# Optimization experiments

Hardware: AMD Instinct MI355X
Metric: run time of the kernel (lower is better)

## Reference

```python
import jax, jax.numpy as jnp
import numpy as np

DIM = 768
NUM_HEADS = 12
MLP_RATIO = 4.0
HIDDEN = int(DIM * MLP_RATIO)
EPS = 1e-6  # flax LayerNorm default


def setup_inputs() -> dict:
    key = jax.random.key(0)
    ks = jax.random.split(key, 8)
    d = DIM
    init = lambda k, shape, fan_in: jax.random.normal(k, shape, jnp.float32) * (fan_in ** -0.5)
    return {
        "x": jax.random.normal(ks[0], (8, 1024, d), jnp.float32),
        "ln1_scale": jnp.ones((d,), jnp.float32),
        "ln1_bias": jnp.zeros((d,), jnp.float32),
        "qkv_w": init(ks[1], (d, 3 * d), d),
        "qkv_b": jnp.zeros((3 * d,), jnp.float32),
        "proj_w": init(ks[2], (d, d), d),
        "proj_b": jnp.zeros((d,), jnp.float32),
        "ln2_scale": jnp.ones((d,), jnp.float32),
        "ln2_bias": jnp.zeros((d,), jnp.float32),
        "fc1_w": init(ks[3], (d, HIDDEN), d),
        "fc1_b": jnp.zeros((HIDDEN,), jnp.float32),
        "fc2_w": init(ks[4], (HIDDEN, d), HIDDEN),
        "fc2_b": jnp.zeros((d,), jnp.float32),
    }


def _layernorm(x, scale, bias):
    mu = jnp.mean(x, axis=-1, keepdims=True)
    var = jnp.mean(jnp.square(x - mu), axis=-1, keepdims=True)
    return (x - mu) * jax.lax.rsqrt(var + EPS) * scale + bias


def reference(x, ln1_scale, ln1_bias, qkv_w, qkv_b, proj_w, proj_b,
              ln2_scale, ln2_bias, fc1_w, fc1_b, fc2_w, fc2_b):
    b, n, d = x.shape
    h = NUM_HEADS
    hd = d // h
    scale = hd ** -0.5

    # --- attention (pre-norm) ---
    y = _layernorm(x, ln1_scale, ln1_bias)
    qkv = y @ qkv_w + qkv_b                      # [b, n, 3d]
    qkv = qkv.reshape(b, n, 3, h, hd).transpose(2, 0, 3, 1, 4)  # [3, b, h, n, hd]
    q, k, v = qkv[0], qkv[1], qkv[2]
    attn = jnp.einsum("bhqd,bhkd->bhqk", q, k) * scale
    attn = jax.nn.softmax(attn, axis=-1)
    o = jnp.einsum("bhqk,bhkd->bhqd", attn, v)   # [b, h, n, hd]
    o = o.transpose(0, 2, 1, 3).reshape(b, n, d)
    x = x + (o @ proj_w + proj_b)

    # --- MLP (pre-norm) ---
    y = _layernorm(x, ln2_scale, ln2_bias)
    y = jax.nn.gelu(y @ fc1_w + fc1_b)
    x = x + (y @ fc2_w + fc2_b)
    return x
```

## Files before the change

### kernel.cpp

```cpp
#include <hip/hip_runtime.h>
#include <hip/hip_bf16.h>
#include <math.h>


#define DIM 768
#define SEQ 1024
#define BATCH 8
#define NHEAD 12
#define HDIM 64
#define HID 3072
#define MTOK (BATCH * SEQ)

typedef __attribute__((ext_vector_type(8))) short short8;
typedef __attribute__((ext_vector_type(4))) short short4v;
typedef __attribute__((ext_vector_type(4))) float floatx4;

__device__ __forceinline__ short f2s(float x) {
  __hip_bfloat16 h = __float2bfloat16(x);
  return __builtin_bit_cast(short, h);
}
__device__ __forceinline__ float s2f(short s) {
  return __bfloat162float(__builtin_bit_cast(__hip_bfloat16, s));
}
__device__ __forceinline__ floatx4 zf4() {
  floatx4 v; v[0] = v[1] = v[2] = v[3] = 0.f; return v;
}
__device__ __forceinline__ float gelu_f(float x) {
  float z = 0.7978845608028654f * (x + 0.044715f * x * x * x);
  float u = __expf(2.f * z);
  return 0.5f * x * (2.f - 2.f / (u + 1.f));
}

__global__ __launch_bounds__(256) void pre_kernel(
    const float* __restrict__ w0, short* __restrict__ o0,
    const float* __restrict__ w1, short* __restrict__ o1,
    const float* __restrict__ w2, short* __restrict__ o2,
    const float* __restrict__ w3, short* __restrict__ o3,
    const float* __restrict__ x, const float* __restrict__ ls,
    const float* __restrict__ lb, short* __restrict__ y) {
  const int id = blockIdx.x;
  const int t = threadIdx.x;
  if (id < 6912) {
    __shared__ float tile[32][33];
    const float* in;
    short* out;
    int K, N, tid;
    if (id < 1728)      { in = w0; out = o0; K = DIM; N = 3 * DIM; tid = id; }
    else if (id < 2304) { in = w1; out = o1; K = DIM; N = DIM;     tid = id - 1728; }
    else if (id < 4608) { in = w2; out = o2; K = DIM; N = HID;     tid = id - 2304; }
    else                { in = w3; out = o3; K = HID; N = DIM;     tid = id - 4608; }
    const int ntx = N >> 5;
    const int n0 = (tid % ntx) * 32, k0 = (tid / ntx) * 32;
    const int tx = t & 31, ty = t >> 5;
#pragma unroll
    for (int i = 0; i < 4; ++i)
      tile[ty + i * 8][tx] = in[(size_t)(k0 + ty + i * 8) * N + n0 + tx];
    __syncthreads();
#pragma unroll
    for (int i = 0; i < 4; ++i)
      out[(size_t)(n0 + ty + i * 8) * K + k0 + tx] = f2s(tile[tx][ty + i * 8]);
  } else {
    const int row = id - 6912;
    const float* xr = x + (size_t)row * DIM;
    float v[3];
    float s1 = 0.f, s2 = 0.f;
#pragma unroll
    for (int j = 0; j < 3; ++j) {
      v[j] = xr[t + j * 256];
      s1 += v[j];
      s2 += v[j] * v[j];
    }
#pragma unroll
    for (int off = 32; off; off >>= 1) {
      s1 += __shfl_down(s1, off, 64);
      s2 += __shfl_down(s2, off, 64);
    }
    __shared__ float r1[4], r2[4], bc[2];
    const int wave = t >> 6, lane = t & 63;
    if (lane == 0) { r1[wave] = s1; r2[wave] = s2; }
    __syncthreads();
    if (t == 0) {
      float S1 = r1[0] + r1[1] + r1[2] + r1[3];
      float S2 = r2[0] + r2[1] + r2[2] + r2[3];
      float mu = S1 * (1.0f / DIM);
      float var = S2 * (1.0f / DIM) - mu * mu;
      bc[0] = mu;
      bc[1] = rsqrtf(fmaxf(var, 0.f) + 1e-6f);
    }
    __syncthreads();
    const float mu = bc[0], rstd = bc[1];
#pragma unroll
    for (int j = 0; j < 3; ++j) {
      const int idx = t + j * 256;
      y[(size_t)row * DIM + idx] = f2s((v[j] - mu) * rstd * ls[idx] + lb[idx]);
    }
  }
}

__global__ __launch_bounds__(256) void ln_kernel(const float* __restrict__ x,
                                                 const float* __restrict__ scale,
                                                 const float* __restrict__ bias,
                                                 short* __restrict__ y) {
  const int row = blockIdx.x;
  const int t = threadIdx.x;
  const float* xr = x + (size_t)row * DIM;
  float v[3];
  float s1 = 0.f, s2 = 0.f;
#pragma unroll
  for (int j = 0; j < 3; ++j) {
    v[j] = xr[t + j * 256];
    s1 += v[j];
    s2 += v[j] * v[j];
  }
#pragma unroll
  for (int off = 32; off; off >>= 1) {
    s1 += __shfl_down(s1, off, 64);
    s2 += __shfl_down(s2, off, 64);
  }
  __shared__ float r1[4], r2[4], bc[2];
  const int wave = t >> 6, lane = t & 63;
  if (lane == 0) { r1[wave] = s1; r2[wave] = s2; }
  __syncthreads();
  if (t == 0) {
    float S1 = r1[0] + r1[1] + r1[2] + r1[3];
    float S2 = r2[0] + r2[1] + r2[2] + r2[3];
    float mu = S1 * (1.0f / DIM);
    float var = S2 * (1.0f / DIM) - mu * mu;
    bc[0] = mu;
    bc[1] = rsqrtf(fmaxf(var, 0.f) + 1e-6f);
  }
  __syncthreads();
  const float mu = bc[0], rstd = bc[1];
#pragma unroll
  for (int j = 0; j < 3; ++j) {
    const int idx = t + j * 256;
    y[(size_t)row * DIM + idx] = f2s((v[j] - mu) * rstd * scale[idx] + bias[idx]);
  }
}

template <int ROWS, int THREADS>
__device__ __forceinline__ void stageT(const short* __restrict__ src, int ld,
                                       short* lds, int t) {
#pragma unroll
  for (int i = 0; i < (ROWS * 4) / THREADS; ++i) {
    const int S = i * THREADS + t;
    const int row = S >> 2;
    const int chunk = (S & 3) ^ ((row >> 1) & 3);
    const short* g = src + (size_t)row * ld + chunk * 8;
    const unsigned off = __builtin_amdgcn_readfirstlane((unsigned)((S & ~63) * 16));
    __builtin_amdgcn_global_load_lds(
        (const __attribute__((address_space(1))) void*)g,
        (__attribute__((address_space(3))) void*)((char*)lds + off), 16, 0, 0);
  }
}

template <int ROWS, int THREADS>
__device__ __forceinline__ void stage8(const short* __restrict__ src, int ld,
                                       short* lds, int t) {
#pragma unroll
  for (int i = 0; i < (ROWS * 8) / THREADS; ++i) {
    const int S = i * THREADS + t;
    const int row = S >> 3;
    const int chunk = (S & 7) ^ (row & 7);
    const short* g = src + (size_t)row * ld + chunk * 8;
    const unsigned off = __builtin_amdgcn_readfirstlane((unsigned)((S & ~63) * 16));
    __builtin_amdgcn_global_load_lds(
        (const __attribute__((address_space(1))) void*)g,
        (__attribute__((address_space(3))) void*)((char*)lds + off), 16, 0, 0);
  }
}

template <int MODE>
__global__ __launch_bounds__(256) void gemm_w192(
    const short* __restrict__ A, const short* __restrict__ Bt,
    const float* __restrict__ bias,
    short* __restrict__ outB,
    short* __restrict__ Qb, short* __restrict__ Kb, short* __restrict__ Vtb,
    int N, int K) {
  __shared__ __align__(16) short Asm[2][4096];
  __shared__ __align__(16) short Bsm[2][6144];
  const int t = threadIdx.x;
  const int lane = t & 63, w = t >> 6, quad = lane >> 4, l15 = lane & 15;

  const int nbx = gridDim.x;
  const int lid = blockIdx.y * nbx + blockIdx.x;
  const int xcd = lid & 7, local = lid >> 3;
  const int m0 = ((local / nbx) * 8 + xcd) * 128;
  const int n0 = (local % nbx) * 192;
  const int mb = (w & 1) * 64, nb = (w >> 1) * 96;

  floatx4 acc[4][6];
#pragma unroll
  for (int mi = 0; mi < 4; ++mi)
#pragma unroll
    for (int ni = 0; ni < 6; ++ni) acc[mi][ni] = zf4();

  stageT<128, 256>(A + (size_t)m0 * K, K, Asm[0], t);
  stageT<192, 256>(Bt + (size_t)n0 * K, K, Bsm[0], t);

  const int nk = K >> 5;
  for (int kt = 0; kt < nk; ++kt) {
    __syncthreads();
    const int cur = kt & 1;
    if (kt + 1 < nk) {
      stageT<128, 256>(A + (size_t)m0 * K + (kt + 1) * 32, K, Asm[cur ^ 1], t);
      stageT<192, 256>(Bt + (size_t)n0 * K + (kt + 1) * 32, K, Bsm[cur ^ 1], t);
    }
    short8 a[4], b[6];
#pragma unroll
    for (int mi = 0; mi < 4; ++mi) {
      const int r = mb + mi * 16 + l15;
      a[mi] = *(const short8*)(Asm[cur] + r * 32 + (quad ^ ((r >> 1) & 3)) * 8);
    }
#pragma unroll
    for (int ni = 0; ni < 6; ++ni) {
      const int r = nb + ni * 16 + l15;
      b[ni] = *(const short8*)(Bsm[cur] + r * 32 + (quad ^ ((r >> 1) & 3)) * 8);
    }
#pragma unroll
    for (int mi = 0; mi < 4; ++mi)
#pragma unroll
      for (int ni = 0; ni < 6; ++ni)
        acc[mi][ni] = __builtin_amdgcn_mfma_f32_16x16x32_bf16(a[mi], b[ni], acc[mi][ni], 0, 0, 0);
  }

#pragma unroll
  for (int mi = 0; mi < 4; ++mi) {
    const int row0 = m0 + mb + mi * 16 + quad * 4;
#pragma unroll
    for (int ni = 0; ni < 6; ++ni) {
      const int col = n0 + nb + ni * 16 + l15;
      const float bv = bias[col];
      float v[4];
#pragma unroll
      for (int r = 0; r < 4; ++r) v[r] = acc[mi][ni][r] + bv;
      if (MODE == 0) {
        const int bb = row0 >> 10;
        const int s0 = row0 & 1023;
        if (col < 1536) {
          const int cc = (col < 768) ? col : col - 768;
          const int h = cc >> 6, d = cc & 63;
          short* dst = (col < 768 ? Qb : Kb) + (size_t)(bb * NHEAD + h) * SEQ * HDIM;
#pragma unroll
          for (int r = 0; r < 4; ++r) dst[(size_t)(s0 + r) * HDIM + d] = f2s(v[r]);
        } else {
          const int cc = col - 1536;
          const int h = cc >> 6, d = cc & 63;
          short4v pv;
#pragma unroll
          for (int r = 0; r < 4; ++r) pv[r] = f2s(v[r]);
          *(short4v*)(Vtb + ((size_t)(bb * NHEAD + h) * HDIM + d) * SEQ + s0) = pv;
        }
      } else {
#pragma unroll
        for (int r = 0; r < 4; ++r)
          outB[(size_t)(row0 + r) * N + col] = f2s(gelu_f(v[r]));
      }
    }
  }
}

__global__ __launch_bounds__(128) void gemm_n64(
    const short* __restrict__ A, const short* __restrict__ Bt,
    const float* __restrict__ bias, const float* __restrict__ res,
    float* __restrict__ outF, int N, int K) {
  __shared__ __align__(16) short Asm[2][8192];
  __shared__ __align__(16) short Bsm[2][4096];
  const int t = threadIdx.x;
  const int lane = t & 63, w = t >> 6, quad = lane >> 4, l15 = lane & 15;

  const int nbx = gridDim.x;
  const int lid = blockIdx.y * nbx + blockIdx.x;
  const int xcd = lid & 7, local = lid >> 3;
  const int m0 = ((local / nbx) * 8 + xcd) * 128;
  const int n0 = (local % nbx) * 64;
  const int mb = w * 64;

  floatx4 acc[4][4];
#pragma unroll
  for (int mi = 0; mi < 4; ++mi)
#pragma unroll
    for (int ni = 0; ni < 4; ++ni) acc[mi][ni] = zf4();

  stage8<128, 128>(A + (size_t)m0 * K, K, Asm[0], t);
  stage8<64, 128>(Bt + (size_t)n0 * K, K, Bsm[0], t);

  const int nk = K >> 6;
  for (int kt = 0; kt < nk; ++kt) {
    __syncthreads();
    const int cur = kt & 1;
    if (kt + 1 < nk) {
      stage8<128, 128>(A + (size_t)m0 * K + (kt + 1) * 64, K, Asm[cur ^ 1], t);
      stage8<64, 128>(Bt + (size_t)n0 * K + (kt + 1) * 64, K, Bsm[cur ^ 1], t);
    }
#pragma unroll
    for (int ks = 0; ks < 2; ++ks) {
      short8 a[4], b[4];
#pragma unroll
      for (int mi = 0; mi < 4; ++mi) {
        const int r = mb + mi * 16 + l15;
        a[mi] = *(const short8*)(Asm[cur] + r * 64 + (((ks * 4 + quad) ^ (r & 7)) * 8));
      }
#pragma unroll
      for (int ni = 0; ni < 4; ++ni) {
        const int r = ni * 16 + l15;
        b[ni] = *(const short8*)(Bsm[cur] + r * 64 + (((ks * 4 + quad) ^ (r & 7)) * 8));
      }
#pragma unroll
      for (int mi = 0; mi < 4; ++mi)
#pragma unroll
        for (int ni = 0; ni < 4; ++ni)
          acc[mi][ni] = __builtin_amdgcn_mfma_f32_16x16x32_bf16(a[mi], b[ni], acc[mi][ni], 0, 0, 0);
    }
  }

#pragma unroll
  for (int mi = 0; mi < 4; ++mi) {
    const int row0 = m0 + mb + mi * 16 + quad * 4;
#pragma unroll
    for (int ni = 0; ni < 4; ++ni) {
      const int col = n0 + ni * 16 + l15;
      const float bv = bias[col];
#pragma unroll
      for (int r = 0; r < 4; ++r) {
        const size_t idx = (size_t)(row0 + r) * N + col;
        outF[idx] = acc[mi][ni][r] + bv + res[idx];
      }
    }
  }
}

__device__ __forceinline__ void stage64(const short* __restrict__ src, int ld,
                                        short* lds, int t) {
  const int lane = t & 63, w = t >> 6;
#pragma unroll
  for (int i = 0; i < 2; ++i) {
    const int S = w * 128 + i * 64 + lane;
    const int r = S >> 3, c0 = S & 7;
    const int c = c0 ^ (r & 7);
    const short* g = src + (size_t)r * ld + c * 8;
    const unsigned off = __builtin_amdgcn_readfirstlane((unsigned)((w * 128 + i * 64) * 16));
    __builtin_amdgcn_global_load_lds(
        (const __attribute__((address_space(1))) void*)g,
        (__attribute__((address_space(3))) void*)((char*)lds + off), 16, 0, 0);
  }
}

__global__ __launch_bounds__(256) void attn_kernel(
    const short* __restrict__ Qb, const short* __restrict__ Kb,
    const short* __restrict__ Vtb, short* __restrict__ o) {
  __shared__ __align__(16) short Ks[2][4096];
  __shared__ __align__(16) short Vts[2][4096];
  __shared__ __align__(16) short Pt[8192];
  const int t = threadIdx.x;
  const int lane = t & 63, w = t >> 6, quad = lane >> 4, l15 = lane & 15;
  const int bh = blockIdx.x;
  const int q0 = blockIdx.y * 128;
  const size_t qkbase = (size_t)bh * SEQ * HDIM;
  const size_t vbase = (size_t)bh * HDIM * SEQ;
  short* ptw = Pt + w * 2048;
  const float cexp = 0.18033688011f;

  short8 bq[2][2];
#pragma unroll
  for (int mi = 0; mi < 2; ++mi)
#pragma unroll
    for (int ks = 0; ks < 2; ++ks)
      bq[mi][ks] = *(const short8*)(Qb + qkbase +
                                    (size_t)(q0 + w * 32 + mi * 16 + l15) * HDIM +
                                    ks * 32 + quad * 8);

  floatx4 oacc[4][2];
  float l_acc[2] = {0.f, 0.f};
#pragma unroll
  for (int di = 0; di < 4; ++di)
#pragma unroll
    for (int mi = 0; mi < 2; ++mi) oacc[di][mi] = zf4();

  stage64(Kb + qkbase, HDIM, Ks[0], t);
  stage64(Vtb + vbase, SEQ, Vts[0], t);

  for (int kt = 0; kt < 16; ++kt) {
    __syncthreads();
    const int cur = kt & 1;
    if (kt < 15) {
      stage64(Kb + qkbase + (size_t)(kt + 1) * 64 * HDIM, HDIM, Ks[cur ^ 1], t);
      stage64(Vtb + vbase + (kt + 1) * 64, SEQ, Vts[cur ^ 1], t);
    }

    floatx4 sacc[4][2];
#pragma unroll
    for (int ni = 0; ni < 4; ++ni)
#pragma unroll
      for (int mi = 0; mi < 2; ++mi) sacc[ni][mi] = zf4();
#pragma unroll
    for (int ks = 0; ks < 2; ++ks) {
      short8 ak[4];
#pragma unroll
      for (int ni = 0; ni < 4; ++ni) {
        const int r = ni * 16 + l15;
        ak[ni] = *(const short8*)(Ks[cur] + r * 64 + (((ks * 4 + quad) ^ (r & 7)) * 8));
      }
#pragma unroll
      for (int ni = 0; ni < 4; ++ni)
#pragma unroll
        for (int mi = 0; mi < 2; ++mi)
          sacc[ni][mi] = __builtin_amdgcn_mfma_f32_16x16x32_bf16(ak[ni], bq[mi][ks], sacc[ni][mi], 0, 0, 0);
    }

#pragma unroll
    for (int mi = 0; mi < 2; ++mi) {
      const int row = mi * 16 + l15;
      const int swz = (row & 7) ^ ((row & 8) >> 1);
#pragma unroll
      for (int ni = 0; ni < 4; ++ni) {
        short4v pk;
#pragma unroll
        for (int r = 0; r < 4; ++r) {
          const float p = exp2f(sacc[ni][mi][r] * cexp);
          l_acc[mi] += p;
          pk[r] = f2s(p);
        }
        const int c = ni * 2 + (quad >> 1);
        *(short4v*)(ptw + row * 64 + ((c ^ swz) * 8 + (quad & 1) * 4)) = pk;
      }
    }

#pragma unroll
    for (int ks = 0; ks < 2; ++ks) {
      short8 bp[2];
#pragma unroll
      for (int mi = 0; mi < 2; ++mi) {
        const int row = mi * 16 + l15;
        const int swz = (row & 7) ^ ((row & 8) >> 1);
        bp[mi] = *(const short8*)(ptw + row * 64 + (((ks * 4 + quad) ^ swz) * 8));
      }
      short8 av[4];
#pragma unroll
      for (int di = 0; di < 4; ++di) {
        const int r = di * 16 + l15;
        av[di] = *(const short8*)(Vts[cur] + r * 64 + (((ks * 4 + quad) ^ (r & 7)) * 8));
      }
#pragma unroll
      for (int di = 0; di < 4; ++di)
#pragma unroll
        for (int mi = 0; mi < 2; ++mi)
          oacc[di][mi] = __builtin_amdgcn_mfma_f32_16x16x32_bf16(av[di], bp[mi], oacc[di][mi], 0, 0, 0);
    }
  }

  const int bb = bh / NHEAD, hh = bh % NHEAD;
  float inv[2];
#pragma unroll
  for (int mi = 0; mi < 2; ++mi) {
    float l = l_acc[mi];
    l += __shfl_xor(l, 16, 64);
    l += __shfl_xor(l, 32, 64);
    inv[mi] = 1.0f / l;
  }
#pragma unroll
  for (int di = 0; di < 4; ++di)
#pragma unroll
    for (int mi = 0; mi < 2; ++mi) {
      const int tok = bb * SEQ + q0 + w * 32 + mi * 16 + l15;
      const int d = hh * HDIM + di * 16 + quad * 4;
      short4v ov;
#pragma unroll
      for (int r = 0; r < 4; ++r) ov[r] = f2s(oacc[di][mi][r] * inv[mi]);
      *(short4v*)(o + (size_t)tok * DIM + d) = ov;
    }
}

extern "C" void kernel_launch(void* const* d_in, const int* in_sizes, int n_in,
                              void* d_out, int out_size, void* d_ws, size_t ws_size,
                              hipStream_t stream) {
  const float* x      = (const float*)d_in[0];
  const float* ln1_s  = (const float*)d_in[1];
  const float* ln1_b  = (const float*)d_in[2];
  const float* qkv_w  = (const float*)d_in[3];
  const float* qkv_b  = (const float*)d_in[4];
  const float* proj_w = (const float*)d_in[5];
  const float* proj_b = (const float*)d_in[6];
  const float* ln2_s  = (const float*)d_in[7];
  const float* ln2_b  = (const float*)d_in[8];
  const float* fc1_w  = (const float*)d_in[9];
  const float* fc1_b  = (const float*)d_in[10];
  const float* fc2_w  = (const float*)d_in[11];
  const float* fc2_b  = (const float*)d_in[12];
  float* out = (float*)d_out;

  char* p = (char*)d_ws;
  short* wqt = (short*)p; p += (size_t)(3 * DIM) * DIM * 2;
  short* wpt = (short*)p; p += (size_t)DIM * DIM * 2;
  short* w1t = (short*)p; p += (size_t)HID * DIM * 2;
  short* w2t = (short*)p; p += (size_t)DIM * HID * 2;
  short* y   = (short*)p; p += (size_t)MTOK * DIM * 2;
  short* Qb  = (short*)p; p += (size_t)MTOK * DIM * 2;
  short* Kb  = (short*)p; p += (size_t)MTOK * DIM * 2;
  short* Vtb = (short*)p; p += (size_t)MTOK * DIM * 2;
  float* x1  = (float*)p; p += (size_t)MTOK * DIM * 4;
  short* h   = (short*)p; p += (size_t)MTOK * HID * 2;
  short* obuf = y;
  short* y2   = Qb;

  pre_kernel<<<6912 + MTOK, 256, 0, stream>>>(qkv_w, wqt, proj_w, wpt, fc1_w, w1t,
                                              fc2_w, w2t, x, ln1_s, ln1_b, y);
  gemm_w192<0><<<dim3(12, 64), 256, 0, stream>>>(
      y, wqt, qkv_b, nullptr, Qb, Kb, Vtb, 3 * DIM, DIM);
  attn_kernel<<<dim3(BATCH * NHEAD, SEQ / 128), 256, 0, stream>>>(Qb, Kb, Vtb, obuf);
  gemm_n64<<<dim3(12, 64), 128, 0, stream>>>(
      obuf, wpt, proj_b, x, x1, DIM, DIM);
  ln_kernel<<<MTOK, 256, 0, stream>>>(x1, ln2_s, ln2_b, y2);
  gemm_w192<2><<<dim3(16, 64), 256, 0, stream>>>(
      y2, w1t, fc1_b, h, nullptr, nullptr, nullptr, HID, DIM);
  gemm_n64<<<dim3(12, 64), 128, 0, stream>>>(
      h, w2t, fc2_b, x1, out, DIM, HID);
}
```

Before: 356.7 us.

## Unify GEMMs into 256x128 triple-buffered 8-wave kernel with split staging

Replaces the two GEMM kernels (a 128x192 tile with 256 threads and a 128x64 tile with 128 threads) with one 512-thread, 256x128-tile GEMM used for all four projections. Global-to-LDS loads are triple-buffered two k-steps ahead, and each k-step is split into two halves with explicit barriers, vmcnt/lgkmcnt waits and s_setprio around the MFMA bursts, so loads interleave with compute. The larger tile raises data reuse per LDS byte. In exchange it launches far fewer blocks (e.g. 192 for proj/fc2) on a 256-CU part, which may underfill the GPU, and the hand-counted wait values risk subtle ordering errors.

```diff
diff --git a/kernel.cpp b/kernel.cpp
--- a/kernel.cpp
+++ b/kernel.cpp
@@ -138,15 +138,15 @@
   }
 }
 
-template <int ROWS, int THREADS>
-__device__ __forceinline__ void stageT(const short* __restrict__ src, int ld,
-                                       short* lds, int t) {
-#pragma unroll
-  for (int i = 0; i < (ROWS * 4) / THREADS; ++i) {
-    const int S = i * THREADS + t;
-    const int row = S >> 2;
-    const int chunk = (S & 3) ^ ((row >> 1) & 3);
-    const short* g = src + (size_t)row * ld + chunk * 8;
+template <int J0, int J1>
+__device__ __forceinline__ void stage512(const short* __restrict__ src, int ldK,
+                                         short* lds, int t) {
+#pragma unroll
+  for (int j = J0; j < J1; ++j) {
+    const int S = j * 512 + t;
+    const int row = S >> 3;
+    const int chunk = (S & 7) ^ (row & 7);
+    const short* g = src + (size_t)row * ldK + chunk * 8;
     const unsigned off = __builtin_amdgcn_readfirstlane((unsigned)((S & ~63) * 16));
     __builtin_amdgcn_global_load_lds(
         (const __attribute__((address_space(1))) void*)g,
@@ -154,82 +154,119 @@
   }
 }
 
-template <int ROWS, int THREADS>
-__device__ __forceinline__ void stage8(const short* __restrict__ src, int ld,
-                                       short* lds, int t) {
-#pragma unroll
-  for (int i = 0; i < (ROWS * 8) / THREADS; ++i) {
-    const int S = i * THREADS + t;
-    const int row = S >> 3;
-    const int chunk = (S & 7) ^ (row & 7);
-    const short* g = src + (size_t)row * ld + chunk * 8;
-    const unsigned off = __builtin_amdgcn_readfirstlane((unsigned)((S & ~63) * 16));
-    __builtin_amdgcn_global_load_lds(
-        (const __attribute__((address_space(1))) void*)g,
-        (__attribute__((address_space(3))) void*)((char*)lds + off), 16, 0, 0);
-  }
-}
-
 template <int MODE>
-__global__ __launch_bounds__(256) void gemm_w192(
+__global__ __launch_bounds__(512) void gemm256(
     const short* __restrict__ A, const short* __restrict__ Bt,
-    const float* __restrict__ bias,
-    short* __restrict__ outB,
+    const float* __restrict__ bias, const float* __restrict__ res,
+    float* __restrict__ outF, short* __restrict__ outB,
     short* __restrict__ Qb, short* __restrict__ Kb, short* __restrict__ Vtb,
     int N, int K) {
-  __shared__ __align__(16) short Asm[2][4096];
-  __shared__ __align__(16) short Bsm[2][6144];
+  __shared__ __align__(16) short Asm[3][16384];
+  __shared__ __align__(16) short Bsm[3][8192];
   const int t = threadIdx.x;
   const int lane = t & 63, w = t >> 6, quad = lane >> 4, l15 = lane & 15;
+  const int wm = w >> 1, wn = w & 1;
 
   const int nbx = gridDim.x;
   const int lid = blockIdx.y * nbx + blockIdx.x;
   const int xcd = lid & 7, local = lid >> 3;
-  const int m0 = ((local / nbx) * 8 + xcd) * 128;
-  const int n0 = (local % nbx) * 192;
-  const int mb = (w & 1) * 64, nb = (w >> 1) * 96;
-
-  floatx4 acc[4][6];
+  const int m0 = ((local / nbx) * 8 + xcd) * 256;
+  const int n0 = (local % nbx) * 128;
+
+  floatx4 acc[4][4];
 #pragma unroll
   for (int mi = 0; mi < 4; ++mi)
 #pragma unroll
-    for (int ni = 0; ni < 6; ++ni) acc[mi][ni] = zf4();
-
-  stageT<128, 256>(A + (size_t)m0 * K, K, Asm[0], t);
-  stageT<192, 256>(Bt + (size_t)n0 * K, K, Bsm[0], t);
-
-  const int nk = K >> 5;
+    for (int ni = 0; ni < 4; ++ni) acc[mi][ni] = zf4();
+
+  const int nk = K >> 6;
+  stage512<0, 4>(A + (size_t)m0 * K, K, Asm[0], t);
+  stage512<0, 2>(Bt + (size_t)n0 * K, K, Bsm[0], t);
+  stage512<0, 4>(A + (size_t)m0 * K + 64, K, Asm[1], t);
+  stage512<0, 2>(Bt + (size_t)n0 * K + 64, K, Bsm[1], t);
+  asm volatile("s_waitcnt vmcnt(6)" ::: "memory");
+  __builtin_amdgcn_s_barrier();
+
+  int sc = 0;
   for (int kt = 0; kt < nk; ++kt) {
-    __syncthreads();
-    const int cur = kt & 1;
-    if (kt + 1 < nk) {
-      stageT<128, 256>(A + (size_t)m0 * K + (kt + 1) * 32, K, Asm[cur ^ 1], t);
-      stageT<192, 256>(Bt + (size_t)n0 * K + (kt + 1) * 32, K, Bsm[cur ^ 1], t);
-    }
-    short8 a[4], b[6];
-#pragma unroll
-    for (int mi = 0; mi < 4; ++mi) {
-      const int r = mb + mi * 16 + l15;
-      a[mi] = *(const short8*)(Asm[cur] + r * 32 + (quad ^ ((r >> 1) & 3)) * 8);
-    }
-#pragma unroll
-    for (int ni = 0; ni < 6; ++ni) {
-      const int r = nb + ni * 16 + l15;
-      b[ni] = *(const short8*)(Bsm[cur] + r * 32 + (quad ^ ((r >> 1) & 3)) * 8);
-    }
-#pragma unroll
-    for (int mi = 0; mi < 4; ++mi)
-#pragma unroll
-      for (int ni = 0; ni < 6; ++ni)
-        acc[mi][ni] = __builtin_amdgcn_mfma_f32_16x16x32_bf16(a[mi], b[ni], acc[mi][ni], 0, 0, 0);
+    int ss = sc + 2; if (ss >= 3) ss -= 3;
+    const short* As = Asm[sc];
+    const short* Bs = Bsm[sc];
+    const bool stg = (kt + 2 < nk);
+    const int koff = (kt + 2) * 64;
+
+    short8 a0[2][2], bf[4][2];
+#pragma unroll
+    for (int mi = 0; mi < 2; ++mi)
+#pragma unroll
+      for (int ks = 0; ks < 2; ++ks) {
+        const int r = wm * 64 + mi * 16 + l15;
+        a0[mi][ks] = *(const short8*)(As + r * 64 + (((ks * 4 + quad) ^ (r & 7)) * 8));
+      }
+#pragma unroll
+    for (int ni = 0; ni < 4; ++ni)
+#pragma unroll
+      for (int ks = 0; ks < 2; ++ks) {
+        const int r = wn * 64 + ni * 16 + l15;
+        bf[ni][ks] = *(const short8*)(Bs + r * 64 + (((ks * 4 + quad) ^ (r & 7)) * 8));
+      }
+    if (stg) {
+      stage512<0, 2>(A + (size_t)m0 * K + koff, K, Asm[ss], t);
+      stage512<0, 1>(Bt + (size_t)n0 * K + koff, K, Bsm[ss], t);
+    }
+    __builtin_amdgcn_s_barrier();
+    asm volatile("s_waitcnt lgkmcnt(0)" ::: "memory");
+    __builtin_amdgcn_s_setprio(1);
+#pragma unroll
+    for (int ks = 0; ks < 2; ++ks)
+#pragma unroll
+      for (int mi = 0; mi < 2; ++mi)
+#pragma unroll
+        for (int ni = 0; ni < 4; ++ni)
+          acc[mi][ni] = __builtin_amdgcn_mfma_f32_16x16x32_bf16(
+              a0[mi][ks], bf[ni][ks], acc[mi][ni], 0, 0, 0);
+    __builtin_amdgcn_s_setprio(0);
+    __builtin_amdgcn_s_barrier();
+
+    short8 a1[2][2];
+#pragma unroll
+    for (int mi = 0; mi < 2; ++mi)
+#pragma unroll
+      for (int ks = 0; ks < 2; ++ks) {
+        const int r = wm * 64 + 32 + mi * 16 + l15;
+        a1[mi][ks] = *(const short8*)(As + r * 64 + (((ks * 4 + quad) ^ (r & 7)) * 8));
+      }
+    if (stg) {
+      stage512<2, 4>(A + (size_t)m0 * K + koff, K, Asm[ss], t);
+      stage512<1, 2>(Bt + (size_t)n0 * K + koff, K, Bsm[ss], t);
+    }
+    __builtin_amdgcn_s_barrier();
+    asm volatile("s_waitcnt lgkmcnt(0)" ::: "memory");
+    __builtin_amdgcn_s_setprio(1);
+#pragma unroll
+    for (int ks = 0; ks < 2; ++ks)
+#pragma unroll
+      for (int mi = 0; mi < 2; ++mi)
+#pragma unroll
+        for (int ni = 0; ni < 4; ++ni)
+          acc[2 + mi][ni] = __builtin_amdgcn_mfma_f32_16x16x32_bf16(
+              a1[mi][ks], bf[ni][ks], acc[2 + mi][ni], 0, 0, 0);
+    __builtin_amdgcn_s_setprio(0);
+    if (stg) {
+      asm volatile("s_waitcnt vmcnt(6)" ::: "memory");
+    } else {
+      asm volatile("s_waitcnt vmcnt(0)" ::: "memory");
+    }
+    __builtin_amdgcn_s_barrier();
+    sc = sc + 1; if (sc == 3) sc = 0;
   }
 
 #pragma unroll
   for (int mi = 0; mi < 4; ++mi) {
-    const int row0 = m0 + mb + mi * 16 + quad * 4;
-#pragma unroll
-    for (int ni = 0; ni < 6; ++ni) {
-      const int col = n0 + nb + ni * 16 + l15;
+    const int row0 = m0 + wm * 64 + mi * 16 + quad * 4;
+#pragma unroll
+    for (int ni = 0; ni < 4; ++ni) {
+      const int col = n0 + wn * 64 + ni * 16 + l15;
       const float bv = bias[col];
       float v[4];
 #pragma unroll
@@ -251,80 +288,16 @@
           for (int r = 0; r < 4; ++r) pv[r] = f2s(v[r]);
           *(short4v*)(Vtb + ((size_t)(bb * NHEAD + h) * HDIM + d) * SEQ + s0) = pv;
         }
+      } else if (MODE == 1) {
+#pragma unroll
+        for (int r = 0; r < 4; ++r) {
+          const size_t idx = (size_t)(row0 + r) * N + col;
+          outF[idx] = v[r] + res[idx];
+        }
       } else {
 #pragma unroll
         for (int r = 0; r < 4; ++r)
           outB[(size_t)(row0 + r) * N + col] = f2s(gelu_f(v[r]));
-      }
-    }
-  }
-}
-
-__global__ __launch_bounds__(128) void gemm_n64(
-    const short* __restrict__ A, const short* __restrict__ Bt,
-    const float* __restrict__ bias, const float* __restrict__ res,
-    float* __restrict__ outF, int N, int K) {
-  __shared__ __align__(16) short Asm[2][8192];
-  __shared__ __align__(16) short Bsm[2][4096];
-  const int t = threadIdx.x;
-  const int lane = t & 63, w = t >> 6, quad = lane >> 4, l15 = lane & 15;
-
-  const int nbx = gridDim.x;
-  const int lid = blockIdx.y * nbx + blockIdx.x;
-  const int xcd = lid & 7, local = lid >> 3;
-  const int m0 = ((local / nbx) * 8 + xcd) * 128;
-  const int n0 = (local % nbx) * 64;
-  const int mb = w * 64;
-
-  floatx4 acc[4][4];
-#pragma unroll
-  for (int mi = 0; mi < 4; ++mi)
-#pragma unroll
-    for (int ni = 0; ni < 4; ++ni) acc[mi][ni] = zf4();
-
-  stage8<128, 128>(A + (size_t)m0 * K, K, Asm[0], t);
-  stage8<64, 128>(Bt + (size_t)n0 * K, K, Bsm[0], t);
-
-  const int nk = K >> 6;
-  for (int kt = 0; kt < nk; ++kt) {
-    __syncthreads();
-    const int cur = kt & 1;
-    if (kt + 1 < nk) {
-      stage8<128, 128>(A + (size_t)m0 * K + (kt + 1) * 64, K, Asm[cur ^ 1], t);
-      stage8<64, 128>(Bt + (size_t)n0 * K + (kt + 1) * 64, K, Bsm[cur ^ 1], t);
-    }
-#pragma unroll
-    for (int ks = 0; ks < 2; ++ks) {
-      short8 a[4], b[4];
-#pragma unroll
-      for (int mi = 0; mi < 4; ++mi) {
-        const int r = mb + mi * 16 + l15;
-        a[mi] = *(const short8*)(Asm[cur] + r * 64 + (((ks * 4 + quad) ^ (r & 7)) * 8));
-      }
-#pragma unroll
-      for (int ni = 0; ni < 4; ++ni) {
-        const int r = ni * 16 + l15;
-        b[ni] = *(const short8*)(Bsm[cur] + r * 64 + (((ks * 4 + quad) ^ (r & 7)) * 8));
-      }
-#pragma unroll
-      for (int mi = 0; mi < 4; ++mi)
-#pragma unroll
-        for (int ni = 0; ni < 4; ++ni)
-          acc[mi][ni] = __builtin_amdgcn_mfma_f32_16x16x32_bf16(a[mi], b[ni], acc[mi][ni], 0, 0, 0);
-    }
-  }
-
-#pragma unroll
-  for (int mi = 0; mi < 4; ++mi) {
-    const int row0 = m0 + mb + mi * 16 + quad * 4;
-#pragma unroll
-    for (int ni = 0; ni < 4; ++ni) {
-      const int col = n0 + ni * 16 + l15;
-      const float bv = bias[col];
-#pragma unroll
-      for (int r = 0; r < 4; ++r) {
-        const size_t idx = (size_t)(row0 + r) * N + col;
-        outF[idx] = acc[mi][ni][r] + bv + res[idx];
       }
     }
   }
@@ -505,14 +478,14 @@
 
   pre_kernel<<<6912 + MTOK, 256, 0, stream>>>(qkv_w, wqt, proj_w, wpt, fc1_w, w1t,
                                               fc2_w, w2t, x, ln1_s, ln1_b, y);
-  gemm_w192<0><<<dim3(12, 64), 256, 0, stream>>>(
-      y, wqt, qkv_b, nullptr, Qb, Kb, Vtb, 3 * DIM, DIM);
+  gemm256<0><<<dim3(18, 32), 512, 0, stream>>>(
+      y, wqt, qkv_b, nullptr, nullptr, nullptr, Qb, Kb, Vtb, 3 * DIM, DIM);
   attn_kernel<<<dim3(BATCH * NHEAD, SEQ / 128), 256, 0, stream>>>(Qb, Kb, Vtb, obuf);
-  gemm_n64<<<dim3(12, 64), 128, 0, stream>>>(
-      obuf, wpt, proj_b, x, x1, DIM, DIM);
+  gemm256<1><<<dim3(6, 32), 512, 0, stream>>>(
+      obuf, wpt, proj_b, x, x1, nullptr, nullptr, nullptr, nullptr, DIM, DIM);
   ln_kernel<<<MTOK, 256, 0, stream>>>(x1, ln2_s, ln2_b, y2);
-  gemm_w192<2><<<dim3(16, 64), 256, 0, stream>>>(
-      y2, w1t, fc1_b, h, nullptr, nullptr, nullptr, HID, DIM);
-  gemm_n64<<<dim3(12, 64), 128, 0, stream>>>(
-      h, w2t, fc2_b, x1, out, DIM, HID);
-}
+  gemm256<2><<<dim3(24, 32), 512, 0, stream>>>(
+      y2, w1t, fc1_b, nullptr, nullptr, h, nullptr, nullptr, nullptr, HID, DIM);
+  gemm256<1><<<dim3(6, 32), 512, 0, stream>>>(
+      h, w2t, fc2_b, x1, out, nullptr, nullptr, nullptr, nullptr, DIM, HID);
+}
```

Result: slower. 365.2 us (+2.4%).

## Deepen GEMM LDS pipelines to four stages with explicit vmcnt waits

Applied to the files above, without the earlier changes.

Both GEMM kernels move from a double-buffered LDS pipeline with __syncthreads to a 4-buffer ring with three K-tiles prefetched ahead. Each iteration waits only for the oldest tile via a partial s_waitcnt vmcnt count before a raw barrier. The n64 kernel also drops its K=64 tile in favour of K=32 tiles with the stageT swizzle. The aim is to hide global-to-LDS load latency better, at the cost of more LDS per block, which may lower occupancy. The hand-counted vmcnt values must exactly match the number of loads issued per stage.

```diff
diff --git a/kernel.cpp b/kernel.cpp
--- a/kernel.cpp
+++ b/kernel.cpp
@@ -154,22 +154,6 @@
   }
 }
 
-template <int ROWS, int THREADS>
-__device__ __forceinline__ void stage8(const short* __restrict__ src, int ld,
-                                       short* lds, int t) {
-#pragma unroll
-  for (int i = 0; i < (ROWS * 8) / THREADS; ++i) {
-    const int S = i * THREADS + t;
-    const int row = S >> 3;
-    const int chunk = (S & 7) ^ (row & 7);
-    const short* g = src + (size_t)row * ld + chunk * 8;
-    const unsigned off = __builtin_amdgcn_readfirstlane((unsigned)((S & ~63) * 16));
-    __builtin_amdgcn_global_load_lds(
-        (const __attribute__((address_space(1))) void*)g,
-        (__attribute__((address_space(3))) void*)((char*)lds + off), 16, 0, 0);
-  }
-}
-
 template <int MODE>
 __global__ __launch_bounds__(256) void gemm_w192(
     const short* __restrict__ A, const short* __restrict__ Bt,
@@ -177,8 +161,8 @@
     short* __restrict__ outB,
     short* __restrict__ Qb, short* __restrict__ Kb, short* __restrict__ Vtb,
     int N, int K) {
-  __shared__ __align__(16) short Asm[2][4096];
-  __shared__ __align__(16) short Bsm[2][6144];
+  __shared__ __align__(16) short Asm[4][4096];
+  __shared__ __align__(16) short Bsm[4][6144];
   const int t = threadIdx.x;
   const int lane = t & 63, w = t >> 6, quad = lane >> 4, l15 = lane & 15;
 
@@ -195,33 +179,46 @@
 #pragma unroll
     for (int ni = 0; ni < 6; ++ni) acc[mi][ni] = zf4();
 
-  stageT<128, 256>(A + (size_t)m0 * K, K, Asm[0], t);
-  stageT<192, 256>(Bt + (size_t)n0 * K, K, Bsm[0], t);
-
+  const short* Ab = A + (size_t)m0 * K;
+  const short* Bb = Bt + (size_t)n0 * K;
   const int nk = K >> 5;
-  for (int kt = 0; kt < nk; ++kt) {
-    __syncthreads();
-    const int cur = kt & 1;
-    if (kt + 1 < nk) {
-      stageT<128, 256>(A + (size_t)m0 * K + (kt + 1) * 32, K, Asm[cur ^ 1], t);
-      stageT<192, 256>(Bt + (size_t)n0 * K + (kt + 1) * 32, K, Bsm[cur ^ 1], t);
-    }
-    short8 a[4], b[6];
-#pragma unroll
-    for (int mi = 0; mi < 4; ++mi) {
-      const int r = mb + mi * 16 + l15;
-      a[mi] = *(const short8*)(Asm[cur] + r * 32 + (quad ^ ((r >> 1) & 3)) * 8);
-    }
-#pragma unroll
-    for (int ni = 0; ni < 6; ++ni) {
-      const int r = nb + ni * 16 + l15;
-      b[ni] = *(const short8*)(Bsm[cur] + r * 32 + (quad ^ ((r >> 1) & 3)) * 8);
-    }
-#pragma unroll
-    for (int mi = 0; mi < 4; ++mi)
-#pragma unroll
-      for (int ni = 0; ni < 6; ++ni)
-        acc[mi][ni] = __builtin_amdgcn_mfma_f32_16x16x32_bf16(a[mi], b[ni], acc[mi][ni], 0, 0, 0);
+
+  stageT<128, 256>(Ab, K, Asm[0], t);       stageT<192, 256>(Bb, K, Bsm[0], t);
+  stageT<128, 256>(Ab + 32, K, Asm[1], t);  stageT<192, 256>(Bb + 32, K, Bsm[1], t);
+  stageT<128, 256>(Ab + 64, K, Asm[2], t);  stageT<192, 256>(Bb + 64, K, Bsm[2], t);
+
+#define W192_STEP(BUF) do { \
+  short8 a_[4], b_[6]; \
+  _Pragma("unroll") for (int mi = 0; mi < 4; ++mi) { \
+    const int r = mb + mi * 16 + l15; \
+    a_[mi] = *(const short8*)(Asm[BUF] + r * 32 + ((quad ^ ((r >> 1) & 3)) * 8)); \
+  } \
+  _Pragma("unroll") for (int ni = 0; ni < 6; ++ni) { \
+    const int r = nb + ni * 16 + l15; \
+    b_[ni] = *(const short8*)(Bsm[BUF] + r * 32 + ((quad ^ ((r >> 1) & 3)) * 8)); \
+  } \
+  _Pragma("unroll") for (int mi = 0; mi < 4; ++mi) \
+    _Pragma("unroll") for (int ni = 0; ni < 6; ++ni) \
+      acc[mi][ni] = __builtin_amdgcn_mfma_f32_16x16x32_bf16(a_[mi], b_[ni], acc[mi][ni], 0, 0, 0); \
+} while (0)
+
+#define W192_IT(J, BUF, NXT) do { \
+  if ((J) + 2 < nk)      asm volatile("s_waitcnt vmcnt(10)" ::: "memory"); \
+  else if ((J) + 1 < nk) asm volatile("s_waitcnt vmcnt(5)" ::: "memory"); \
+  else                   asm volatile("s_waitcnt vmcnt(0)" ::: "memory"); \
+  __builtin_amdgcn_s_barrier(); \
+  if ((J) + 3 < nk) { \
+    stageT<128, 256>(Ab + ((J) + 3) * 32, K, Asm[NXT], t); \
+    stageT<192, 256>(Bb + ((J) + 3) * 32, K, Bsm[NXT], t); \
+  } \
+  W192_STEP(BUF); \
+} while (0)
+
+  for (int kt = 0; kt < nk; kt += 4) {
+    W192_IT(kt + 0, 0, 3);
+    W192_IT(kt + 1, 1, 0);
+    W192_IT(kt + 2, 2, 1);
+    W192_IT(kt + 3, 3, 2);
   }
 
 #pragma unroll
@@ -264,8 +261,8 @@
     const short* __restrict__ A, const short* __restrict__ Bt,
     const float* __restrict__ bias, const float* __restrict__ res,
     float* __restrict__ outF, int N, int K) {
-  __shared__ __align__(16) short Asm[2][8192];
-  __shared__ __align__(16) short Bsm[2][4096];
+  __shared__ __align__(16) short Asm[4][4096];
+  __shared__ __align__(16) short Bsm[4][2048];
   const int t = threadIdx.x;
   const int lane = t & 63, w = t >> 6, quad = lane >> 4, l15 = lane & 15;
 
@@ -282,36 +279,46 @@
 #pragma unroll
     for (int ni = 0; ni < 4; ++ni) acc[mi][ni] = zf4();
 
-  stage8<128, 128>(A + (size_t)m0 * K, K, Asm[0], t);
-  stage8<64, 128>(Bt + (size_t)n0 * K, K, Bsm[0], t);
-
-  const int nk = K >> 6;
-  for (int kt = 0; kt < nk; ++kt) {
-    __syncthreads();
-    const int cur = kt & 1;
-    if (kt + 1 < nk) {
-      stage8<128, 128>(A + (size_t)m0 * K + (kt + 1) * 64, K, Asm[cur ^ 1], t);
-      stage8<64, 128>(Bt + (size_t)n0 * K + (kt + 1) * 64, K, Bsm[cur ^ 1], t);
-    }
-#pragma unroll
-    for (int ks = 0; ks < 2; ++ks) {
-      short8 a[4], b[4];
-#pragma unroll
-      for (int mi = 0; mi < 4; ++mi) {
-        const int r = mb + mi * 16 + l15;
-        a[mi] = *(const short8*)(Asm[cur] + r * 64 + (((ks * 4 + quad) ^ (r & 7)) * 8));
-      }
-#pragma unroll
-      for (int ni = 0; ni < 4; ++ni) {
-        const int r = ni * 16 + l15;
-        b[ni] = *(const short8*)(Bsm[cur] + r * 64 + (((ks * 4 + quad) ^ (r & 7)) * 8));
-      }
-#pragma unroll
-      for (int mi = 0; mi < 4; ++mi)
-#pragma unroll
-        for (int ni = 0; ni < 4; ++ni)
-          acc[mi][ni] = __builtin_amdgcn_mfma_f32_16x16x32_bf16(a[mi], b[ni], acc[mi][ni], 0, 0, 0);
-    }
+  const short* Ab = A + (size_t)m0 * K;
+  const short* Bb = Bt + (size_t)n0 * K;
+  const int nk = K >> 5;
+
+  stageT<128, 128>(Ab, K, Asm[0], t);       stageT<64, 128>(Bb, K, Bsm[0], t);
+  stageT<128, 128>(Ab + 32, K, Asm[1], t);  stageT<64, 128>(Bb + 32, K, Bsm[1], t);
+  stageT<128, 128>(Ab + 64, K, Asm[2], t);  stageT<64, 128>(Bb + 64, K, Bsm[2], t);
+
+#define N64_STEP(BUF) do { \
+  short8 a_[4], b_[4]; \
+  _Pragma("unroll") for (int mi = 0; mi < 4; ++mi) { \
+    const int r = mb + mi * 16 + l15; \
+    a_[mi] = *(const short8*)(Asm[BUF] + r * 32 + ((quad ^ ((r >> 1) & 3)) * 8)); \
+  } \
+  _Pragma("unroll") for (int ni = 0; ni < 4; ++ni) { \
+    const int r = ni * 16 + l15; \
+    b_[ni] = *(const short8*)(Bsm[BUF] + r * 32 + ((quad ^ ((r >> 1) & 3)) * 8)); \
+  } \
+  _Pragma("unroll") for (int mi = 0; mi < 4; ++mi) \
+    _Pragma("unroll") for (int ni = 0; ni < 4; ++ni) \
+      acc[mi][ni] = __builtin_amdgcn_mfma_f32_16x16x32_bf16(a_[mi], b_[ni], acc[mi][ni], 0, 0, 0); \
+} while (0)
+
+#define N64_IT(J, BUF, NXT) do { \
+  if ((J) + 2 < nk)      asm volatile("s_waitcnt vmcnt(12)" ::: "memory"); \
+  else if ((J) + 1 < nk) asm volatile("s_waitcnt vmcnt(6)" ::: "memory"); \
+  else                   asm volatile("s_waitcnt vmcnt(0)" ::: "memory"); \
+  __builtin_amdgcn_s_barrier(); \
+  if ((J) + 3 < nk) { \
+    stageT<128, 128>(Ab + ((J) + 3) * 32, K, Asm[NXT], t); \
+    stageT<64, 128>(Bb + ((J) + 3) * 32, K, Bsm[NXT], t); \
+  } \
+  N64_STEP(BUF); \
+} while (0)
+
+  for (int kt = 0; kt < nk; kt += 4) {
+    N64_IT(kt + 0, 0, 3);
+    N64_IT(kt + 1, 1, 0);
+    N64_IT(kt + 2, 2, 1);
+    N64_IT(kt + 3, 3, 2);
   }
 
 #pragma unroll
```

After: 423.1 us. 1.19x slower.

## Load GEMM A-operand fragments directly from global into registers, bypassing LDS

Applied to the files above, without the earlier changes.

In both GEMM kernels, each wave now loads its A-operand MFMA fragments straight from global memory into registers, double-buffered across k-steps. Only the B tile is still staged through LDS, and the k-loop is unrolled by two so the two buffers alternate with fixed indices. This removes the A LDS staging, its LDS footprint and the LDS reads, which may raise occupancy. In exchange, the global A loads are less coalesced (16-byte strided row reads), waves sharing A rows fetch them redundantly, more registers are live, and the loop assumes nk is even.

```diff
diff --git a/kernel.cpp b/kernel.cpp
--- a/kernel.cpp
+++ b/kernel.cpp
@@ -177,7 +177,6 @@
     short* __restrict__ outB,
     short* __restrict__ Qb, short* __restrict__ Kb, short* __restrict__ Vtb,
     int N, int K) {
-  __shared__ __align__(16) short Asm[2][4096];
   __shared__ __align__(16) short Bsm[2][6144];
   const int t = threadIdx.x;
   const int lane = t & 63, w = t >> 6, quad = lane >> 4, l15 = lane & 15;
@@ -189,39 +188,49 @@
   const int n0 = (local % nbx) * 192;
   const int mb = (w & 1) * 64, nb = (w >> 1) * 96;
 
+  const short* pa[4];
+#pragma unroll
+  for (int mi = 0; mi < 4; ++mi)
+    pa[mi] = A + (size_t)(m0 + mb + mi * 16 + l15) * K + quad * 8;
+
   floatx4 acc[4][6];
 #pragma unroll
   for (int mi = 0; mi < 4; ++mi)
 #pragma unroll
     for (int ni = 0; ni < 6; ++ni) acc[mi][ni] = zf4();
 
-  stageT<128, 256>(A + (size_t)m0 * K, K, Asm[0], t);
+#define W192_STEP(BUF, AR) do { \
+  short8 b_[6]; \
+  _Pragma("unroll") for (int ni = 0; ni < 6; ++ni) { \
+    const int r = nb + ni * 16 + l15; \
+    b_[ni] = *(const short8*)(Bsm[BUF] + r * 32 + ((quad ^ ((r >> 1) & 3)) * 8)); \
+  } \
+  _Pragma("unroll") for (int mi = 0; mi < 4; ++mi) \
+    _Pragma("unroll") for (int ni = 0; ni < 6; ++ni) \
+      acc[mi][ni] = __builtin_amdgcn_mfma_f32_16x16x32_bf16(AR[mi], b_[ni], acc[mi][ni], 0, 0, 0); \
+} while (0)
+
+  short8 a0[4], a1[4];
+#pragma unroll
+  for (int mi = 0; mi < 4; ++mi) a0[mi] = *(const short8*)(pa[mi]);
   stageT<192, 256>(Bt + (size_t)n0 * K, K, Bsm[0], t);
 
   const int nk = K >> 5;
-  for (int kt = 0; kt < nk; ++kt) {
-    __syncthreads();
-    const int cur = kt & 1;
-    if (kt + 1 < nk) {
-      stageT<128, 256>(A + (size_t)m0 * K + (kt + 1) * 32, K, Asm[cur ^ 1], t);
-      stageT<192, 256>(Bt + (size_t)n0 * K + (kt + 1) * 32, K, Bsm[cur ^ 1], t);
-    }
-    short8 a[4], b[6];
-#pragma unroll
-    for (int mi = 0; mi < 4; ++mi) {
-      const int r = mb + mi * 16 + l15;
-      a[mi] = *(const short8*)(Asm[cur] + r * 32 + (quad ^ ((r >> 1) & 3)) * 8);
-    }
-#pragma unroll
-    for (int ni = 0; ni < 6; ++ni) {
-      const int r = nb + ni * 16 + l15;
-      b[ni] = *(const short8*)(Bsm[cur] + r * 32 + (quad ^ ((r >> 1) & 3)) * 8);
-    }
+  for (int kt = 0; kt < nk; kt += 2) {
+    __syncthreads();
+    stageT<192, 256>(Bt + (size_t)n0 * K + (kt + 1) * 32, K, Bsm[1], t);
 #pragma unroll
     for (int mi = 0; mi < 4; ++mi)
-#pragma unroll
-      for (int ni = 0; ni < 6; ++ni)
-        acc[mi][ni] = __builtin_amdgcn_mfma_f32_16x16x32_bf16(a[mi], b[ni], acc[mi][ni], 0, 0, 0);
+      a1[mi] = *(const short8*)(pa[mi] + (kt + 1) * 32);
+    W192_STEP(0, a0);
+    __syncthreads();
+    if (kt + 2 < nk) {
+      stageT<192, 256>(Bt + (size_t)n0 * K + (kt + 2) * 32, K, Bsm[0], t);
+#pragma unroll
+      for (int mi = 0; mi < 4; ++mi)
+        a0[mi] = *(const short8*)(pa[mi] + (kt + 2) * 32);
+    }
+    W192_STEP(1, a1);
   }
 
 #pragma unroll
@@ -264,7 +273,6 @@
     const short* __restrict__ A, const short* __restrict__ Bt,
     const float* __restrict__ bias, const float* __restrict__ res,
     float* __restrict__ outF, int N, int K) {
-  __shared__ __align__(16) short Asm[2][8192];
   __shared__ __align__(16) short Bsm[2][4096];
   const int t = threadIdx.x;
   const int lane = t & 63, w = t >> 6, quad = lane >> 4, l15 = lane & 15;
@@ -276,42 +284,52 @@
   const int n0 = (local % nbx) * 64;
   const int mb = w * 64;
 
+  const short* pa[4];
+#pragma unroll
+  for (int mi = 0; mi < 4; ++mi)
+    pa[mi] = A + (size_t)(m0 + mb + mi * 16 + l15) * K + quad * 8;
+
   floatx4 acc[4][4];
 #pragma unroll
   for (int mi = 0; mi < 4; ++mi)
 #pragma unroll
     for (int ni = 0; ni < 4; ++ni) acc[mi][ni] = zf4();
 
-  stage8<128, 128>(A + (size_t)m0 * K, K, Asm[0], t);
+#define N64_LOADA(AR, KOFF) do { \
+  _Pragma("unroll") for (int ks = 0; ks < 2; ++ks) \
+    _Pragma("unroll") for (int mi = 0; mi < 4; ++mi) \
+      AR[ks * 4 + mi] = *(const short8*)(pa[mi] + (KOFF) + ks * 32); \
+} while (0)
+
+#define N64_STEP(BUF, AR) do { \
+  _Pragma("unroll") for (int ks = 0; ks < 2; ++ks) { \
+    short8 b_[4]; \
+    _Pragma("unroll") for (int ni = 0; ni < 4; ++ni) { \
+      const int r = ni * 16 + l15; \
+      b_[ni] = *(const short8*)(Bsm[BUF] + r * 64 + (((ks * 4 + quad) ^ (r & 7)) * 8)); \
+    } \
+    _Pragma("unroll") for (int mi = 0; mi < 4; ++mi) \
+      _Pragma("unroll") for (int ni = 0; ni < 4; ++ni) \
+        acc[mi][ni] = __builtin_amdgcn_mfma_f32_16x16x32_bf16(AR[ks * 4 + mi], b_[ni], acc[mi][ni], 0, 0, 0); \
+  } \
+} while (0)
+
+  short8 a0[8], a1[8];
+  N64_LOADA(a0, 0);
   stage8<64, 128>(Bt + (size_t)n0 * K, K, Bsm[0], t);
 
   const int nk = K >> 6;
-  for (int kt = 0; kt < nk; ++kt) {
-    __syncthreads();
-    const int cur = kt & 1;
-    if (kt + 1 < nk) {
-      stage8<128, 128>(A + (size_t)m0 * K + (kt + 1) * 64, K, Asm[cur ^ 1], t);
-      stage8<64, 128>(Bt + (size_t)n0 * K + (kt + 1) * 64, K, Bsm[cur ^ 1], t);
-    }
-#pragma unroll
-    for (int ks = 0; ks < 2; ++ks) {
-      short8 a[4], b[4];
-#pragma unroll
-      for (int mi = 0; mi < 4; ++mi) {
-        const int r = mb + mi * 16 + l15;
-        a[mi] = *(const short8*)(Asm[cur] + r * 64 + (((ks * 4 + quad) ^ (r & 7)) * 8));
-      }
-#pragma unroll
-      for (int ni = 0; ni < 4; ++ni) {
-        const int r = ni * 16 + l15;
-        b[ni] = *(const short8*)(Bsm[cur] + r * 64 + (((ks * 4 + quad) ^ (r & 7)) * 8));
-      }
-#pragma unroll
-      for (int mi = 0; mi < 4; ++mi)
-#pragma unroll
-        for (int ni = 0; ni < 4; ++ni)
-          acc[mi][ni] = __builtin_amdgcn_mfma_f32_16x16x32_bf16(a[mi], b[ni], acc[mi][ni], 0, 0, 0);
-    }
+  for (int kt = 0; kt < nk; kt += 2) {
+    __syncthreads();
+    stage8<64, 128>(Bt + (size_t)n0 * K + (kt + 1) * 64, K, Bsm[1], t);
+    N64_LOADA(a1, (kt + 1) * 64);
+    N64_STEP(0, a0);
+    __syncthreads();
+    if (kt + 2 < nk) {
+      stage8<64, 128>(Bt + (size_t)n0 * K + (kt + 2) * 64, K, Bsm[0], t);
+      N64_LOADA(a0, (kt + 2) * 64);
+    }
+    N64_STEP(1, a1);
   }
 
 #pragma unroll
```

Measured after the change: 470.5 us. +31.9%, slower.
